# Kernel optimization log

Hardware: AMD Instinct MI355X
Metric: run time of the kernel (lower is better)

Reference implementation:

```python
import jax, jax.numpy as jnp
import numpy as np

B, N, F_IN = 32, 1024, 64   # batch, num_nodes, diffusion_size[0]
K = 3                        # expansion_step
H = 2                        # num_heads
HID, RAW, OUT, CLS = 128, 128, 128, 2
D1, D2 = 128, 128            # diffusion_size[1], diffusion_size[2]
CAT = D1 + RAW               # concat dim fed to attention (h || h_prime) = 256


def setup_inputs() -> dict:
    key = jax.random.key(0)
    ks = jax.random.split(key, 40)
    g = lambda i, shape: jax.random.normal(ks[i], shape, dtype=jnp.float32) * 0.05
    inp = {
        'X': jax.random.normal(ks[0], (B, N, F_IN), dtype=jnp.float32),
        'A': jax.random.uniform(ks[1], (B, N, N), dtype=jnp.float32),
        # transition tensors / mixing weights (only the 2 layers used in forward)
        'T': g(2, (2, K, N, N)),
        'theta': jnp.full((2, K), 1.0 / K, dtype=jnp.float32),
        # raw feature projection
        'W_raw': g(3, (F_IN, RAW)), 'b_raw': jnp.zeros((RAW,), jnp.float32),
        # diffusion layer linears
        'Wd0': g(4, (F_IN, D1)), 'bd0': jnp.zeros((D1,), jnp.float32),
        'Wd1': g(5, (D1, D2)),   'bd1': jnp.zeros((D2,), jnp.float32),
        # final classifier
        'W_fin': g(6, (OUT, CLS)), 'b_fin': jnp.zeros((CLS,), jnp.float32),
    }
    # two CatMultiAttn blocks: q/k/v projections (CAT->HID), out proj (HID->OUT)
    i = 7
    for l in range(2):
        for nm in ('q', 'k', 'v'):
            inp[f'W{nm}{l}'] = g(i, (CAT, HID)); i += 1
            inp[f'b{nm}{l}'] = jnp.zeros((HID,), jnp.float32)
        inp[f'Wo{l}'] = g(i, (HID, OUT)); i += 1
        inp[f'bo{l}'] = jnp.zeros((OUT,), jnp.float32)
    return inp


def _diffusion(theta_l, T_l, h, A, W, b):
    # Q = sum_k theta_k * T_k  (generalized graph diffusion transition)
    Q = jnp.einsum('k,kij->ij', theta_l, T_l)          # [N,N]
    S = Q[None, :, :] * A                               # [B,N,N] mask by adjacency
    z = jnp.einsum('bij,bjf->bif', S, h)                # diffuse features
    return jax.nn.relu(z @ W + b)


def _cat_attn(h, hp, Wq, bq, Wk, bk, Wv, bv, Wo, bo):
    # concatenate diffused + embedding features, multi-head self-attn over nodes
    x = jnp.concatenate([h, hp], axis=-1)               # [B,N,CAT]
    b, n, _ = x.shape
    q = (x @ Wq + bq).reshape(b, n, H, HID // H)
    k = (x @ Wk + bk).reshape(b, n, H, HID // H)
    v = (x @ Wv + bv).reshape(b, n, H, HID // H)
    scale = jnp.asarray(1.0 / np.sqrt(HID // H), x.dtype)
    s = jnp.einsum('bnhd,bmhd->bhnm', q, k) * scale     # [B,H,N,N]
    p = jax.nn.softmax(s, axis=-1)
    ctx = jnp.einsum('bhnm,bmhd->bnhd', p, v).reshape(b, n, HID)
    return jax.nn.relu(ctx @ Wo + bo)


def reference(X, A, T, theta, W_raw, b_raw, Wd0, bd0, Wd1, bd1,
              W_fin, b_fin,
              Wq0, bq0, Wk0, bk0, Wv0, bv0, Wo0, bo0,
              Wq1, bq1, Wk1, bk1, Wv1, bv1, Wo1, bo1):
    theta_soft = jax.nn.softmax(theta, axis=-1)         # [2,K]
    h_prime = X @ W_raw + b_raw                          # [B,N,RAW]
    # layer 0
    h = _diffusion(theta_soft[0], T[0], X, A, Wd0, bd0)  # [B,N,D1]
    h_prime = _cat_attn(h, h_prime, Wq0, bq0, Wk0, bk0, Wv0, bv0, Wo0, bo0)
    # layer 1 (residual fusion)
    h = _diffusion(theta_soft[1], T[1], h, A, Wd1, bd1)  # [B,N,D2]
    h_prime = h_prime + _cat_attn(h, h_prime, Wq1, bq1, Wk1, bk1, Wv1, bv1, Wo1, bo1)
    return h_prime @ W_fin + b_fin                       # [B,N,CLS]
```

## Files before the change

kernel.cpp:

```cpp
#include <hip/hip_runtime.h>
#include <hip/hip_bf16.h>

typedef __hip_bfloat16 bf16;
typedef __attribute__((ext_vector_type(8))) short s8b;
typedef __attribute__((ext_vector_type(4))) short s4b;
typedef __attribute__((ext_vector_type(4))) float f4;
typedef __attribute__((ext_vector_type(4))) float fv4;

#define BB   32
#define NN   1024
#define FIN  64
#define HEADS 2
#define DH   64
#define HIDD 128
#define SZQ  ((size_t)BB * NN * HIDD)

__device__ __forceinline__ ushort f2bf(float x) {
    bf16 h = __float2bfloat16(x);
    return *(ushort*)&h;
}
__device__ __forceinline__ float bfbits2f(ushort h) {
    union { uint u; float f; } c; c.u = (uint)h << 16; return c.f;
}
__device__ __forceinline__ uint pk_bf16(float lo, float hi) {
    return (uint)f2bf(lo) | ((uint)f2bf(hi) << 16);
}
union U8 { short s[8]; s8b v; };
union U4 { short s[4]; s4b v; };
union UQ { ushort u[8]; s8b v; };

__global__ __launch_bounds__(256) void setup_kernel(
        const float* __restrict__ raw, const float* __restrict__ d0,
        const float* __restrict__ d1,
        const float* __restrict__ q0w, const float* __restrict__ k0w,
        const float* __restrict__ v0w, const float* __restrict__ o0w,
        const float* __restrict__ q1w, const float* __restrict__ k1w,
        const float* __restrict__ v1w, const float* __restrict__ o1w,
        ushort* __restrict__ Whi, ushort* __restrict__ Wlo,
        const float* __restrict__ T, const float* __restrict__ theta,
        ushort* __restrict__ Q0hi, ushort* __restrict__ Q0lo,
        ushort* __restrict__ Q1hi, ushort* __restrict__ Q1lo,
        const float* __restrict__ X,
        ushort* __restrict__ XT_hi, ushort* __restrict__ XT_lo) {
    __shared__ float tile[64][65];
    const int bid = blockIdx.x;
    const int t = threadIdx.x;
    if (bid < 1024) {
        int id = bid * 256 + t;
        const float* src; int K, off;
        if      (id <   8192) { src = raw; K =  64; off = 0; }
        else if (id <  16384) { src = d0;  K =  64; off = 8192; }
        else if (id <  32768) { src = d1;  K = 128; off = 16384; }
        else if (id <  65536) { src = q0w; K = 256; off = 32768; }
        else if (id <  98304) { src = k0w; K = 256; off = 65536; }
        else if (id < 131072) { src = v0w; K = 256; off = 98304; }
        else if (id < 147456) { src = o0w; K = 128; off = 131072; }
        else if (id < 180224) { src = q1w; K = 256; off = 147456; }
        else if (id < 212992) { src = k1w; K = 256; off = 180224; }
        else if (id < 245760) { src = v1w; K = 256; off = 212992; }
        else                  { src = o1w; K = 128; off = 245760; }
        int il = id - off;
        int k = il >> 7, c = il & 127;
        float w = src[il];
        ushort h = f2bf(w);
        Whi[off + c * K + k] = h;
        Wlo[off + c * K + k] = f2bf(w - bfbits2f(h));
    } else if (bid < 1536) {
        const int tb = bid - 1024;
        const int b  = tb >> 4;
        const int n0 = (tb & 15) * 64;
        {
            int nl = t >> 2, f0 = (t & 3) * 16;
            const float* xp = X + ((size_t)b * NN + n0 + nl) * 64 + f0;
#pragma unroll
            for (int i = 0; i < 16; i += 4)
                *(float4*)&tile[nl][f0 + i] = *(const float4*)(xp + i);
        }
        __syncthreads();
        {
            int f = t >> 2, n1 = (t & 3) * 16;
            U8 h0, h1, l0, l1;
#pragma unroll
            for (int i = 0; i < 16; i++) {
                float v = tile[n1 + i][f];
                ushort hh = f2bf(v);
                ushort ll = f2bf(v - bfbits2f(hh));
                if (i < 8) { h0.s[i] = (short)hh; l0.s[i] = (short)ll; }
                else       { h1.s[i - 8] = (short)hh; l1.s[i - 8] = (short)ll; }
            }
            size_t gb = ((size_t)b * 64 + f) * NN + n0 + n1;
            *(s8b*)&XT_hi[gb]     = h0.v;  *(s8b*)&XT_hi[gb + 8] = h1.v;
            *(s8b*)&XT_lo[gb]     = l0.v;  *(s8b*)&XT_lo[gb + 8] = l1.v;
        }
    } else {
        const int layer = (bid < 2048) ? 0 : 1;
        ushort* Qhi = layer ? Q1hi : Q0hi;
        ushort* Qlo = layer ? Q1lo : Q0lo;
        float t0 = theta[layer * 3 + 0];
        float t1 = theta[layer * 3 + 1];
        float t2 = theta[layer * 3 + 2];
        float m  = fmaxf(t0, fmaxf(t1, t2));
        float e0 = expf(t0 - m), e1 = expf(t1 - m), e2 = expf(t2 - m);
        float inv = 1.0f / (e0 + e1 + e2);
        e0 *= inv; e1 *= inv; e2 *= inv;
        size_t base = ((size_t)((bid - 1536) & 511) * 256 + t) * 8;
        const float* Tl = T + (size_t)layer * 3 * NN * NN;
        U8 hi, lo;
#pragma unroll
        for (int i = 0; i < 8; i++) {
            float q = e0 * Tl[base + i]
                    + e1 * Tl[base + i + (size_t)NN * NN]
                    + e2 * Tl[base + i + (size_t)2 * NN * NN];
            ushort hh = f2bf(q);
            hi.s[i] = (short)hh;
            lo.s[i] = (short)f2bf(q - bfbits2f(hh));
        }
        *(s8b*)&Qhi[base] = hi.v;
        *(s8b*)&Qlo[base] = lo.v;
    }
}

template<int F, bool WRITE_HT>
__global__ __launch_bounds__(512, 4) void diff_dense_kernel(
        const ushort* __restrict__ Qhi, const ushort* __restrict__ Qlo,
        const float* __restrict__ A,
        const ushort* __restrict__ hT_hi, const ushort* __restrict__ hT_lo,
        const ushort* __restrict__ WT_hi, const ushort* __restrict__ WT_lo,
        const float* __restrict__ bias,
        float* __restrict__ hout,
        ushort* __restrict__ hiT, ushort* __restrict__ loT) {
    constexpr int SS  = 72;
    constexpr int NT  = F / 16;
    constexpr int NCW = NT / 4;
    constexpr int SZ2 = F + 8;
    constexpr int P1 = 2 * 64 * SS + 2 * F * SS;
    constexpr int P2 = 2 * 64 * SZ2 + 2 * 128 * 40;
    __shared__ short smem[(P1 > P2) ? P1 : P2];
    short* Shi = smem;
    short* Slo = Shi + 64 * SS;
    short* Hhi = Slo + 64 * SS;
    short* Hlo = Hhi + (size_t)F * SS;
    short* Zhi = smem;
    short* Zlo = Zhi + 64 * SZ2;
    short* Wsh = Zlo + 64 * SZ2;
    short* Wsl = Wsh + 128 * 40;

    const int bidx = blockIdx.x;
    const int u  = bidx >> 3;
    const int b  = (bidx & 7) + 8 * (u >> 4);
    const int i0 = (u & 15) * 64;
    const int t  = threadIdx.x;
    const int w  = t >> 6, lane = t & 63;
    const int quad = lane >> 4, c = lane & 15;
    const int rh = w >> 2;
    const int ch = w & 3;

    const int srow = t >> 3, scol = (t & 7) * 8;
    const float*  Ap = A   + ((size_t)b * NN + i0 + srow) * NN + scol;
    const ushort* Qh = Qhi + (size_t)(i0 + srow) * NN + scol;
    const ushort* Ql = Qlo + (size_t)(i0 + srow) * NN + scol;
    constexpr int HTR = 512 / F;
    constexpr int HJ  = 64 / HTR;
    constexpr int HV  = HJ / 8;
    const int hrow = t / HTR, hcol = (t % HTR) * HJ;
    const ushort* Hh = hT_hi + ((size_t)b * F + hrow) * NN + hcol;
    const ushort* Hl = hT_lo + ((size_t)b * F + hrow) * NN + hcol;

    f4 acc[2][NCW];
#pragma unroll
    for (int i = 0; i < 2; i++)
#pragma unroll
        for (int j = 0; j < NCW; j++) acc[i][j] = (f4){0.f, 0.f, 0.f, 0.f};

    fv4 a0 = __builtin_nontemporal_load((const fv4*)Ap);
    fv4 a1 = __builtin_nontemporal_load((const fv4*)(Ap + 4));
    s8b hhv[HV], hlv[HV];
#pragma unroll
    for (int vv = 0; vv < HV; vv++) {
        hhv[vv] = *(const s8b*)(Hh + 8 * vv);
        hlv[vv] = *(const s8b*)(Hl + 8 * vv);
    }
    UQ qh, ql;
    qh.v = *(const s8b*)Qh;
    ql.v = *(const s8b*)Ql;

#pragma unroll 1
    for (int j0 = 0; j0 < NN; j0 += 64) {
        __syncthreads();
        {
            float av[8] = {a0[0], a0[1], a0[2], a0[3], a1[0], a1[1], a1[2], a1[3]};
            U8 hi, lo;
#pragma unroll
            for (int i = 0; i < 8; i++) {
                float q = bfbits2f(qh.u[i]) + bfbits2f(ql.u[i]);
                float s = q * av[i];
                ushort hb = f2bf(s);
                hi.s[i] = (short)hb;
                lo.s[i] = (short)f2bf(s - bfbits2f(hb));
            }
            *(s8b*)&Shi[srow * SS + scol] = hi.v;
            *(s8b*)&Slo[srow * SS + scol] = lo.v;
#pragma unroll
            for (int vv = 0; vv < HV; vv++) {
                *(s8b*)&Hhi[hrow * SS + hcol + 8 * vv] = hhv[vv];
                *(s8b*)&Hlo[hrow * SS + hcol + 8 * vv] = hlv[vv];
            }
        }
        __syncthreads();

        if (j0 + 64 < NN) {
            a0 = __builtin_nontemporal_load((const fv4*)(Ap + j0 + 64));
            a1 = __builtin_nontemporal_load((const fv4*)(Ap + j0 + 68));
#pragma unroll
            for (int vv = 0; vv < HV; vv++) {
                hhv[vv] = *(const s8b*)(Hh + j0 + 64 + 8 * vv);
                hlv[vv] = *(const s8b*)(Hl + j0 + 64 + 8 * vv);
            }
            qh.v = *(const s8b*)(Qh + j0 + 64);
            ql.v = *(const s8b*)(Ql + j0 + 64);
        }

#pragma unroll
        for (int ks = 0; ks < 2; ks++) {
            s8b ah0 = *(const s8b*)&Shi[(32 * rh + c) * SS + ks * 32 + quad * 8];
            s8b al0 = *(const s8b*)&Slo[(32 * rh + c) * SS + ks * 32 + quad * 8];
            s8b ah1 = *(const s8b*)&Shi[(32 * rh + 16 + c) * SS + ks * 32 + quad * 8];
            s8b al1 = *(const s8b*)&Slo[(32 * rh + 16 + c) * SS + ks * 32 + quad * 8];
#pragma unroll
            for (int ctn = 0; ctn < NCW; ctn++) {
                const int nt = ch * NCW + ctn;
                s8b bhi = *(const s8b*)&Hhi[(nt * 16 + c) * SS + ks * 32 + quad * 8];
                s8b blo = *(const s8b*)&Hlo[(nt * 16 + c) * SS + ks * 32 + quad * 8];
                acc[0][ctn] = __builtin_amdgcn_mfma_f32_16x16x32_bf16(ah0, bhi, acc[0][ctn], 0, 0, 0);
                acc[0][ctn] = __builtin_amdgcn_mfma_f32_16x16x32_bf16(al0, bhi, acc[0][ctn], 0, 0, 0);
                acc[0][ctn] = __builtin_amdgcn_mfma_f32_16x16x32_bf16(ah0, blo, acc[0][ctn], 0, 0, 0);
                acc[1][ctn] = __builtin_amdgcn_mfma_f32_16x16x32_bf16(ah1, bhi, acc[1][ctn], 0, 0, 0);
                acc[1][ctn] = __builtin_amdgcn_mfma_f32_16x16x32_bf16(al1, bhi, acc[1][ctn], 0, 0, 0);
                acc[1][ctn] = __builtin_amdgcn_mfma_f32_16x16x32_bf16(ah1, blo, acc[1][ctn], 0, 0, 0);
            }
        }
    }

    __syncthreads();
#pragma unroll
    for (int st = 0; st < 2; st++)
#pragma unroll
        for (int ctn = 0; ctn < NCW; ctn++)
#pragma unroll
            for (int r = 0; r < 4; r++) {
                const int row = 32 * rh + 16 * st + quad * 4 + r;
                const int col = (ch * NCW + ctn) * 16 + c;
                float v = acc[st][ctn][r];
                ushort hh = f2bf(v);
                Zhi[row * SZ2 + col] = (short)hh;
                Zlo[row * SZ2 + col] = (short)f2bf(v - bfbits2f(hh));
            }

    const int rh2 = w >> 2;
    const int ch2 = w & 3;
    f4 acc2[2][2];
#pragma unroll
    for (int st = 0; st < 2; st++)
#pragma unroll
        for (int i = 0; i < 2; i++) acc2[st][i] = (f4){0.f, 0.f, 0.f, 0.f};

    constexpr int NKT = F / 32;
    const int wcc = t >> 2, wkk = (t & 3) * 8;
    s8b pwh = *(const s8b*)&WT_hi[(size_t)wcc * F + wkk];
    s8b pwl = *(const s8b*)&WT_lo[(size_t)wcc * F + wkk];
    for (int kt = 0; kt < NKT; kt++) {
        __syncthreads();
        *(s8b*)&Wsh[wcc * 40 + wkk] = pwh;
        *(s8b*)&Wsl[wcc * 40 + wkk] = pwl;
        __syncthreads();
        if (kt + 1 < NKT) {
            size_t gsrc = (size_t)wcc * F + (kt + 1) * 32 + wkk;
            pwh = *(const s8b*)&WT_hi[gsrc];
            pwl = *(const s8b*)&WT_lo[gsrc];
        }

        s8b ah0 = *(const s8b*)&Zhi[(32 * rh2 + c) * SZ2 + kt * 32 + quad * 8];
        s8b al0 = *(const s8b*)&Zlo[(32 * rh2 + c) * SZ2 + kt * 32 + quad * 8];
        s8b ah1 = *(const s8b*)&Zhi[(32 * rh2 + 16 + c) * SZ2 + kt * 32 + quad * 8];
        s8b al1 = *(const s8b*)&Zlo[(32 * rh2 + 16 + c) * SZ2 + kt * 32 + quad * 8];
#pragma unroll
        for (int ct = 0; ct < 2; ct++) {
            s8b bh = *(const s8b*)&Wsh[(ch2 * 32 + ct * 16 + c) * 40 + quad * 8];
            s8b bl = *(const s8b*)&Wsl[(ch2 * 32 + ct * 16 + c) * 40 + quad * 8];
            acc2[0][ct] = __builtin_amdgcn_mfma_f32_16x16x32_bf16(ah0, bh, acc2[0][ct], 0, 0, 0);
            acc2[0][ct] = __builtin_amdgcn_mfma_f32_16x16x32_bf16(al0, bh, acc2[0][ct], 0, 0, 0);
            acc2[0][ct] = __builtin_amdgcn_mfma_f32_16x16x32_bf16(ah0, bl, acc2[0][ct], 0, 0, 0);
            acc2[1][ct] = __builtin_amdgcn_mfma_f32_16x16x32_bf16(ah1, bh, acc2[1][ct], 0, 0, 0);
            acc2[1][ct] = __builtin_amdgcn_mfma_f32_16x16x32_bf16(al1, bh, acc2[1][ct], 0, 0, 0);
            acc2[1][ct] = __builtin_amdgcn_mfma_f32_16x16x32_bf16(ah1, bl, acc2[1][ct], 0, 0, 0);
        }
    }

#pragma unroll
    for (int st = 0; st < 2; st++) {
        const int rg0 = i0 + 32 * rh2 + 16 * st + quad * 4;
#pragma unroll
        for (int ct = 0; ct < 2; ct++) {
            const int col = ch2 * 32 + ct * 16 + c;
            float bv = bias[col];
            float vv[4];
#pragma unroll
            for (int r = 0; r < 4; r++) {
                float v = fmaxf(acc2[st][ct][r] + bv, 0.f);
                hout[((size_t)b * NN + rg0 + r) * 128 + col] = v;
                vv[r] = v;
            }
            if (WRITE_HT) {
                U4 ph, pl;
#pragma unroll
                for (int r = 0; r < 4; r++) {
                    ushort hh = f2bf(vv[r]);
                    ph.s[r] = (short)hh;
                    pl.s[r] = (short)f2bf(vv[r] - bfbits2f(hh));
                }
                size_t tb = ((size_t)b * 128 + col) * NN + rg0;
                *(s4b*)&hiT[tb] = ph.v;
                *(s4b*)&loT[tb] = pl.v;
            }
        }
    }
}

template<int K1, int K2, int CB, bool RELU, bool RESID, int OMODE>
__global__ __launch_bounds__(512) void dense_mfma_kernel(
        const float* __restrict__ in1, const float* __restrict__ in2,
        const ushort* __restrict__ WT_hi, const ushort* __restrict__ WT_lo,
        const float* __restrict__ bias, const float* __restrict__ biask,
        const float* __restrict__ biasv,
        float* __restrict__ out, ushort* __restrict__ outq) {
    constexpr int KD  = K1 + K2;
    constexpr int NKT = KD / 32;
    constexpr int NCH = CB / 32;
    constexpr int WCH = CB * 4;
    constexpr int WPT = (WCH + 511) / 512;
    __shared__ short Xhi[128][40], Xlo[128][40];
    __shared__ short Whi[CB][40], Wlo[CB][40];

    int bx, by;
    if (OMODE == 1) {
        const int xcd = blockIdx.x & 7, qq = blockIdx.x >> 3;
        by = qq & 1;
        bx = ((qq >> 1) << 3) | xcd;
    } else { bx = blockIdx.x; by = blockIdx.y; }
    const int r0 = bx * 128;
    const int c0 = by * CB;
    const int t  = threadIdx.x;
    const int w  = t >> 6, lane = t & 63;
    const int quad = lane >> 4, c = lane & 15;
    const int rh = w >> 1;
    const int ch = w & 1;

    f4 acc[2][NCH];
#pragma unroll
    for (int st = 0; st < 2; st++)
#pragma unroll
        for (int i = 0; i < NCH; i++) acc[st][i] = (f4){0.f, 0.f, 0.f, 0.f};

    const int xrow = t >> 2, xkk = (t & 3) * 8;
    float4 pa, pbq;
    s8b pwh[WPT], pwl[WPT];
    auto loadX = [&](int k0) {
        int g = r0 + xrow;
        const float* p;
        if (K2 > 0) {
            int k = k0 + xkk;
            p = (k < K1) ? (in1 + (size_t)g * K1 + k)
                         : (in2 + (size_t)g * K2 + (k - K1));
        } else {
            p = in1 + (size_t)g * K1 + k0 + xkk;
        }
        pa = *(const float4*)p; pbq = *(const float4*)(p + 4);
    };
    auto loadW = [&](int k0) {
#pragma unroll
        for (int i = 0; i < WPT; i++) {
            int id = t + i * 512;
            if ((WCH % 512 == 0) || id < WCH) {
                int cc = id >> 2, kk = (id & 3) * 8;
                size_t gsrc = (size_t)(c0 + cc) * KD + k0 + kk;
                pwh[i] = *(const s8b*)&WT_hi[gsrc];
                pwl[i] = *(const s8b*)&WT_lo[gsrc];
            }
        }
    };
    loadX(0); loadW(0);

    for (int kt = 0; kt < NKT; kt++) {
        __syncthreads();
        {
            float sv[8] = {pa.x, pa.y, pa.z, pa.w, pbq.x, pbq.y, pbq.z, pbq.w};
            U8 hi, lo;
#pragma unroll
            for (int i = 0; i < 8; i++) {
                ushort hh = f2bf(sv[i]);
                hi.s[i] = (short)hh;
                lo.s[i] = (short)f2bf(sv[i] - bfbits2f(hh));
            }
            *(s8b*)&Xhi[xrow][xkk] = hi.v;
            *(s8b*)&Xlo[xrow][xkk] = lo.v;
        }
        {
#pragma unroll
            for (int i = 0; i < WPT; i++) {
                int id = t + i * 512;
                if ((WCH % 512 == 0) || id < WCH) {
                    int cc = id >> 2, kk = (id & 3) * 8;
                    *(s8b*)&Whi[cc][kk] = pwh[i];
                    *(s8b*)&Wlo[cc][kk] = pwl[i];
                }
            }
        }
        __syncthreads();
        if (kt + 1 < NKT) { loadX(kt * 32 + 32); loadW(kt * 32 + 32); }

        s8b ah0 = *(const s8b*)&Xhi[32 * rh + c][quad * 8];
        s8b al0 = *(const s8b*)&Xlo[32 * rh + c][quad * 8];
        s8b ah1 = *(const s8b*)&Xhi[32 * rh + 16 + c][quad * 8];
        s8b al1 = *(const s8b*)&Xlo[32 * rh + 16 + c][quad * 8];
#pragma unroll
        for (int ct = 0; ct < NCH; ct++) {
            s8b bh = *(const s8b*)&Whi[ch * (CB / 2) + ct * 16 + c][quad * 8];
            s8b bl = *(const s8b*)&Wlo[ch * (CB / 2) + ct * 16 + c][quad * 8];
            acc[0][ct] = __builtin_amdgcn_mfma_f32_16x16x32_bf16(ah0, bh, acc[0][ct], 0, 0, 0);
            acc[0][ct] = __builtin_amdgcn_mfma_f32_16x16x32_bf16(al0, bh, acc[0][ct], 0, 0, 0);
            acc[0][ct] = __builtin_amdgcn_mfma_f32_16x16x32_bf16(ah0, bl, acc[0][ct], 0, 0, 0);
            acc[1][ct] = __builtin_amdgcn_mfma_f32_16x16x32_bf16(ah1, bh, acc[1][ct], 0, 0, 0);
            acc[1][ct] = __builtin_amdgcn_mfma_f32_16x16x32_bf16(al1, bh, acc[1][ct], 0, 0, 0);
            acc[1][ct] = __builtin_amdgcn_mfma_f32_16x16x32_bf16(ah1, bl, acc[1][ct], 0, 0, 0);
        }
    }

#pragma unroll
    for (int st = 0; st < 2; st++) {
        const int row_g0 = r0 + 32 * rh + 16 * st + quad * 4;
#pragma unroll
        for (int ct = 0; ct < NCH; ct++) {
            const int col = c0 + ch * (CB / 2) + ct * 16 + c;
            if (OMODE == 1) {
                int tensor = col >> 7, cc2 = col & 127;
                float bv = (tensor == 0 ? bias : tensor == 1 ? biask : biasv)[cc2];
                int head = cc2 >> 6, d = cc2 & 63;
                int b = row_g0 >> 10, n = row_g0 & 1023;
                if (tensor == 2) {
                    U4 pk;
#pragma unroll
                    for (int r = 0; r < 4; r++) pk.s[r] = (short)f2bf(acc[st][ct][r] + bv);
                    size_t addr = (((size_t)b * HEADS + head) * 64 + d) * NN + n;
                    *(s4b*)&outq[2 * SZQ + addr] = pk.v;
                } else {
                    ushort* dst = outq + (size_t)tensor * SZQ
                                + (((size_t)b * HEADS + head) * NN + n) * 64 + d;
#pragma unroll
                    for (int r = 0; r < 4; r++) dst[(size_t)r * 64] = f2bf(acc[st][ct][r] + bv);
                }
            } else {
                float bv = bias[col];
#pragma unroll
                for (int r = 0; r < 4; r++) {
                    float v = acc[st][ct][r] + bv;
                    if (RELU) v = fmaxf(v, 0.f);
                    size_t o = (size_t)(row_g0 + r) * 128 + col;
                    if (RESID) v += out[o];
                    out[o] = v;
                }
            }
        }
    }
}

template<bool FINAL>
__global__ __launch_bounds__(512) void attn_oproj_kernel(
        const ushort* __restrict__ q, const ushort* __restrict__ k,
        const ushort* __restrict__ vt,
        const ushort* __restrict__ WoT_hi, const ushort* __restrict__ WoT_lo,
        const float* __restrict__ bo,
        float* __restrict__ hp,
        const float* __restrict__ Wfin, const float* __restrict__ bfin,
        float* __restrict__ fout) {
    constexpr int ZS = 136;
    constexpr int PB = 2 * 128 * ZS + 2 * 128 * 40 + 512;
    __shared__ short smem[PB];
    short* Ks  = smem;
    short* Vt  = smem + 128 * 72;
    short* Zhi = smem;
    short* Zlo = Zhi + 128 * ZS;
    short* Wsh = Zlo + 128 * ZS;
    short* Wsl = Wsh + 128 * 40;
    float* red = (float*)(Wsl + 128 * 40);

    const int bidx = blockIdx.x;
    const int u  = bidx >> 3;
    const int b  = (bidx & 7) + 8 * (u >> 3);
    const int n0 = (u & 7) * 128;
    const int t  = threadIdx.x;
    const int w  = t >> 6;
    const int lane = t & 63;
    const int quad = lane >> 4, c = lane & 15;
    const float scale = 0.125f;

    const int skey = t >> 2, sd0 = (t & 3) * 16;
    const int svd  = t >> 3, svc = (t & 7) * 16;

    s8b pk0, pk1, pv0, pv1;
    auto loadKV = [&](size_t base, int kt0) {
        const ushort* kr = k + base + (size_t)(kt0 + skey) * 64 + sd0;
        pk0 = *(const s8b*)kr;
        pk1 = *(const s8b*)(kr + 8);
        const ushort* vr = vt + base + (size_t)svd * NN + kt0 + svc;
        pv0 = *(const s8b*)vr;
        pv1 = *(const s8b*)(vr + 8);
    };

    f4 Oh[2][4];
    float li[2];

#pragma unroll
    for (int h = 0; h < 2; h++) {
        const size_t kvbase = ((size_t)(b * HEADS + h)) * NN * 64;
        s8b qf0, qf1;
        {
            const ushort* qrow = q + kvbase + (size_t)(n0 + 16 * w + c) * 64;
            qf0 = *(const s8b*)(qrow + quad * 8);
            qf1 = *(const s8b*)(qrow + 32 + quad * 8);
        }
        if (h == 0) loadKV(kvbase, 0);
        f4 O[4];
#pragma unroll
        for (int i = 0; i < 4; i++) O[i] = (f4){0.f, 0.f, 0.f, 0.f};
        float l_i = 0.f;

        for (int kt0 = 0; kt0 < NN; kt0 += 128) {
            __syncthreads();
            {
                *(s8b*)&Ks[skey * 72 + sd0]     = pk0;
                *(s8b*)&Ks[skey * 72 + sd0 + 8] = pk1;
                *(s8b*)&Vt[svd * 136 + svc]     = pv0;
                *(s8b*)&Vt[svd * 136 + svc + 8] = pv1;
            }
            __syncthreads();
            if (kt0 + 128 < NN)      loadKV(kvbase, kt0 + 128);
            else if (h == 0)         loadKV(kvbase + (size_t)NN * 64, 0);

            f4 sg[4][2];
#pragma unroll
            for (int g = 0; g < 4; g++) {
                const int kb = g * 32;
                sg[g][0] = (f4){0.f, 0.f, 0.f, 0.f};
                sg[g][1] = (f4){0.f, 0.f, 0.f, 0.f};
#pragma unroll
                for (int ck = 0; ck < 2; ck++) {
                    s8b ka = *(const s8b*)&Ks[(kb + c) * 72 + ck * 32 + quad * 8];
                    s8b kB = *(const s8b*)&Ks[(kb + 16 + c) * 72 + ck * 32 + quad * 8];
                    s8b qf = ck ? qf1 : qf0;
                    sg[g][0] = __builtin_amdgcn_mfma_f32_16x16x32_bf16(ka, qf, sg[g][0], 0, 0, 0);
                    sg[g][1] = __builtin_amdgcn_mfma_f32_16x16x32_bf16(kB, qf, sg[g][1], 0, 0, 0);
                }
            }
            float pv[4][8];
            float ps = 0.f;
#pragma unroll
            for (int g = 0; g < 4; g++)
#pragma unroll
                for (int r = 0; r < 4; r++) {
                    pv[g][r]     = __expf(sg[g][0][r] * scale);
                    pv[g][4 + r] = __expf(sg[g][1][r] * scale);
                    ps += pv[g][r] + pv[g][4 + r];
                }
            ps += __shfl_xor(ps, 16);
            ps += __shfl_xor(ps, 32);
            l_i += ps;

            int addr0 = ((((2 * quad) & 3) << 4) | c) << 2;
            int addr1 = ((((2 * quad + 1) & 3) << 4) | c) << 2;
            int tsel = quad >> 1;
#pragma unroll
            for (int g = 0; g < 4; g++) {
                const int kb = g * 32;
                uint Da01 = pk_bf16(pv[g][0], pv[g][1]), Da23 = pk_bf16(pv[g][2], pv[g][3]);
                uint Db01 = pk_bf16(pv[g][4], pv[g][5]), Db23 = pk_bf16(pv[g][6], pv[g][7]);
                int A01_0 = __builtin_amdgcn_ds_bpermute(addr0, (int)Da01);
                int A23_0 = __builtin_amdgcn_ds_bpermute(addr0, (int)Da23);
                int B01_0 = __builtin_amdgcn_ds_bpermute(addr0, (int)Db01);
                int B23_0 = __builtin_amdgcn_ds_bpermute(addr0, (int)Db23);
                int A01_1 = __builtin_amdgcn_ds_bpermute(addr1, (int)Da01);
                int A23_1 = __builtin_amdgcn_ds_bpermute(addr1, (int)Da23);
                int B01_1 = __builtin_amdgcn_ds_bpermute(addr1, (int)Db01);
                int B23_1 = __builtin_amdgcn_ds_bpermute(addr1, (int)Db23);
                union { int i[4]; s8b s; } pf;
                pf.i[0] = tsel ? B01_0 : A01_0;
                pf.i[1] = tsel ? B23_0 : A23_0;
                pf.i[2] = tsel ? B01_1 : A01_1;
                pf.i[3] = tsel ? B23_1 : A23_1;
#pragma unroll
                for (int dt = 0; dt < 4; dt++) {
                    s8b vf = *(const s8b*)&Vt[(16 * dt + c) * 136 + kb + quad * 8];
                    O[dt] = __builtin_amdgcn_mfma_f32_16x16x32_bf16(vf, pf.s, O[dt], 0, 0, 0);
                }
            }
        }
        li[h] = 1.0f / l_i;
#pragma unroll
        for (int dt = 0; dt < 4; dt++) Oh[h][dt] = O[dt];
    }

    __syncthreads();
    {
        const int zrow = 16 * w + c;
#pragma unroll
        for (int h = 0; h < 2; h++) {
            float inv = li[h];
#pragma unroll
            for (int dt = 0; dt < 4; dt++) {
                U4 ph, pl;
#pragma unroll
                for (int r = 0; r < 4; r++) {
                    float v = Oh[h][dt][r] * inv;
                    ushort hh = f2bf(v);
                    ph.s[r] = (short)hh;
                    pl.s[r] = (short)f2bf(v - bfbits2f(hh));
                }
                int col = h * 64 + 16 * dt + 4 * quad;
                *(s4b*)&Zhi[zrow * ZS + col] = ph.v;
                *(s4b*)&Zlo[zrow * ZS + col] = pl.v;
            }
        }
    }

    const int rh = w >> 1;
    const int ch = w & 1;
    f4 acc[2][4];
#pragma unroll
    for (int st = 0; st < 2; st++)
#pragma unroll
        for (int i = 0; i < 4; i++) acc[st][i] = (f4){0.f, 0.f, 0.f, 0.f};

    const int occ = t >> 2, okk = (t & 3) * 8;
    s8b owh = *(const s8b*)&WoT_hi[(size_t)occ * 128 + okk];
    s8b owl = *(const s8b*)&WoT_lo[(size_t)occ * 128 + okk];
    for (int kt = 0; kt < 4; kt++) {
        __syncthreads();
        *(s8b*)&Wsh[occ * 40 + okk] = owh;
        *(s8b*)&Wsl[occ * 40 + okk] = owl;
        __syncthreads();
        if (kt + 1 < 4) {
            size_t gsrc = (size_t)occ * 128 + (kt + 1) * 32 + okk;
            owh = *(const s8b*)&WoT_hi[gsrc];
            owl = *(const s8b*)&WoT_lo[gsrc];
        }

        s8b ah0 = *(const s8b*)&Zhi[(32 * rh + c) * ZS + kt * 32 + quad * 8];
        s8b al0 = *(const s8b*)&Zlo[(32 * rh + c) * ZS + kt * 32 + quad * 8];
        s8b ah1 = *(const s8b*)&Zhi[(32 * rh + 16 + c) * ZS + kt * 32 + quad * 8];
        s8b al1 = *(const s8b*)&Zlo[(32 * rh + 16 + c) * ZS + kt * 32 + quad * 8];
#pragma unroll
        for (int ct = 0; ct < 4; ct++) {
            s8b bh = *(const s8b*)&Wsh[(ch * 64 + ct * 16 + c) * 40 + quad * 8];
            s8b bl = *(const s8b*)&Wsl[(ch * 64 + ct * 16 + c) * 40 + quad * 8];
            acc[0][ct] = __builtin_amdgcn_mfma_f32_16x16x32_bf16(ah0, bh, acc[0][ct], 0, 0, 0);
            acc[0][ct] = __builtin_amdgcn_mfma_f32_16x16x32_bf16(al0, bh, acc[0][ct], 0, 0, 0);
            acc[0][ct] = __builtin_amdgcn_mfma_f32_16x16x32_bf16(ah0, bl, acc[0][ct], 0, 0, 0);
            acc[1][ct] = __builtin_amdgcn_mfma_f32_16x16x32_bf16(ah1, bh, acc[1][ct], 0, 0, 0);
            acc[1][ct] = __builtin_amdgcn_mfma_f32_16x16x32_bf16(al1, bh, acc[1][ct], 0, 0, 0);
            acc[1][ct] = __builtin_amdgcn_mfma_f32_16x16x32_bf16(ah1, bl, acc[1][ct], 0, 0, 0);
        }
    }

    if (FINAL) {
        float fc[2][2][4];
#pragma unroll
        for (int st = 0; st < 2; st++)
#pragma unroll
            for (int o = 0; o < 2; o++)
#pragma unroll
                for (int r = 0; r < 4; r++) fc[st][o][r] = 0.f;
#pragma unroll
        for (int ct = 0; ct < 4; ct++) {
            const int col = ch * 64 + ct * 16 + c;
            float bv = bo[col];
            float w0 = Wfin[col * 2], w1 = Wfin[col * 2 + 1];
#pragma unroll
            for (int st = 0; st < 2; st++) {
                const size_t rg = (size_t)b * NN + n0 + 32 * rh + 16 * st + quad * 4;
#pragma unroll
                for (int r = 0; r < 4; r++) {
                    float v = fmaxf(acc[st][ct][r] + bv, 0.f);
                    v += hp[(rg + r) * 128 + col];
                    fc[st][0][r] += v * w0;
                    fc[st][1][r] += v * w1;
                }
            }
        }
#pragma unroll
        for (int st = 0; st < 2; st++)
#pragma unroll
            for (int r = 0; r < 4; r++) {
                float a0 = fc[st][0][r], a1 = fc[st][1][r];
#pragma unroll
                for (int off = 1; off < 16; off <<= 1) {
                    a0 += __shfl_xor(a0, off, 16);
                    a1 += __shfl_xor(a1, off, 16);
                }
                fc[st][0][r] = a0; fc[st][1][r] = a1;
            }
        if (ch == 1 && c == 0) {
#pragma unroll
            for (int st = 0; st < 2; st++)
#pragma unroll
                for (int r = 0; r < 4; r++) {
                    int lr = 32 * rh + 16 * st + quad * 4 + r;
                    red[lr * 2]     = fc[st][0][r];
                    red[lr * 2 + 1] = fc[st][1][r];
                }
        }
        __syncthreads();
        if (ch == 0 && c == 0) {
#pragma unroll
            for (int st = 0; st < 2; st++)
#pragma unroll
                for (int r = 0; r < 4; r++) {
                    int lr = 32 * rh + 16 * st + quad * 4 + r;
                    size_t row = (size_t)b * NN + n0 + lr;
                    fout[row * 2]     = fc[st][0][r] + red[lr * 2]     + bfin[0];
                    fout[row * 2 + 1] = fc[st][1][r] + red[lr * 2 + 1] + bfin[1];
                }
        }
        return;
    }

#pragma unroll
    for (int st = 0; st < 2; st++) {
        const size_t rg = (size_t)b * NN + n0 + 32 * rh + 16 * st + quad * 4;
#pragma unroll
        for (int ct = 0; ct < 4; ct++) {
            const int col = ch * 64 + ct * 16 + c;
            float bv = bo[col];
#pragma unroll
            for (int r = 0; r < 4; r++)
                hp[(rg + r) * 128 + col] = fmaxf(acc[st][ct][r] + bv, 0.f);
        }
    }
}

extern "C" void kernel_launch(void* const* d_in, const int* in_sizes, int n_in,
                              void* d_out, int out_size, void* d_ws, size_t ws_size,
                              hipStream_t stream) {
    (void)in_sizes; (void)n_in; (void)out_size; (void)ws_size;
    const float* X     = (const float*)d_in[0];
    const float* A     = (const float*)d_in[1];
    const float* T     = (const float*)d_in[2];
    const float* theta = (const float*)d_in[3];
    const float* W_raw = (const float*)d_in[4];
    const float* b_raw = (const float*)d_in[5];
    const float* Wd0   = (const float*)d_in[6];
    const float* bd0   = (const float*)d_in[7];
    const float* Wd1   = (const float*)d_in[8];
    const float* bd1   = (const float*)d_in[9];
    const float* W_fin = (const float*)d_in[10];
    const float* b_fin = (const float*)d_in[11];
    const float* Wq0 = (const float*)d_in[12]; const float* bq0 = (const float*)d_in[13];
    const float* Wk0 = (const float*)d_in[14]; const float* bk0 = (const float*)d_in[15];
    const float* Wv0 = (const float*)d_in[16]; const float* bv0 = (const float*)d_in[17];
    const float* Wo0 = (const float*)d_in[18]; const float* bo0 = (const float*)d_in[19];
    const float* Wq1 = (const float*)d_in[20]; const float* bq1 = (const float*)d_in[21];
    const float* Wk1 = (const float*)d_in[22]; const float* bk1 = (const float*)d_in[23];
    const float* Wv1 = (const float*)d_in[24]; const float* bv1 = (const float*)d_in[25];
    const float* Wo1 = (const float*)d_in[26]; const float* bo1 = (const float*)d_in[27];

    float* ws   = (float*)d_ws;
    const size_t SZ = (size_t)BB * NN * HIDD;
    ushort* Q0hi = (ushort*)ws;
    ushort* Q0lo = Q0hi + (size_t)NN * NN;
    float* hp   = ws + (size_t)NN * NN;
    float* h    = hp + SZ;
    float* z    = h + SZ;
    ushort* qb  = (ushort*)(z + SZ);
    ushort* kb  = qb + SZ;
    ushort* XT_hi = qb + 3 * SZ;
    ushort* XT_lo = XT_hi + SZ / 2;
    ushort* hT_hi = XT_lo + SZ / 2;
    ushort* hT_lo = hT_hi + SZ;
    ushort* WT_hi = hT_lo + SZ;
    ushort* WT_lo = WT_hi + 262144;
    ushort* Q1hi = WT_lo + 262144;
    ushort* Q1lo = Q1hi + (size_t)NN * NN;

    const int OFF_RAW = 0, OFF_D0 = 8192, OFF_D1 = 16384, OFF_QKV0 = 32768,
              OFF_O0 = 131072, OFF_QKV1 = 147456, OFF_O1 = 245760;

    const int attnGrid = BB * (NN / 128);
    const int diffGrid = BB * (NN / 64);
    const dim3 dg1(256, 1);

    setup_kernel<<<2560, 256, 0, stream>>>(W_raw, Wd0, Wd1, Wq0, Wk0, Wv0, Wo0,
                                           Wq1, Wk1, Wv1, Wo1, WT_hi, WT_lo,
                                           T, theta, Q0hi, Q0lo, Q1hi, Q1lo,
                                           X, XT_hi, XT_lo);

    dense_mfma_kernel<64, 0, 128, false, false, 0><<<dg1, 512, 0, stream>>>(
        X, nullptr, WT_hi + OFF_RAW, WT_lo + OFF_RAW, b_raw, nullptr, nullptr,
        hp, nullptr);
    diff_dense_kernel<64, true><<<diffGrid, 512, 0, stream>>>(
        Q0hi, Q0lo, A, XT_hi, XT_lo, WT_hi + OFF_D0, WT_lo + OFF_D0, bd0,
        h, hT_hi, hT_lo);
    dense_mfma_kernel<128, 128, 192, false, false, 1><<<512, 512, 0, stream>>>(
        h, hp, WT_hi + OFF_QKV0, WT_lo + OFF_QKV0, bq0, bk0, bv0,
        nullptr, qb);
    attn_oproj_kernel<false><<<attnGrid, 512, 0, stream>>>(
        qb, kb, qb + 2 * SZ, WT_hi + OFF_O0, WT_lo + OFF_O0, bo0,
        hp, nullptr, nullptr, nullptr);

    diff_dense_kernel<128, false><<<diffGrid, 512, 0, stream>>>(
        Q1hi, Q1lo, A, hT_hi, hT_lo, WT_hi + OFF_D1, WT_lo + OFF_D1, bd1,
        h, nullptr, nullptr);
    dense_mfma_kernel<128, 128, 192, false, false, 1><<<512, 512, 0, stream>>>(
        h, hp, WT_hi + OFF_QKV1, WT_lo + OFF_QKV1, bq1, bk1, bv1,
        nullptr, qb);
    attn_oproj_kernel<true><<<attnGrid, 512, 0, stream>>>(
        qb, kb, qb + 2 * SZ, WT_hi + OFF_O1, WT_lo + OFF_O1, bo1,
        hp, W_fin, b_fin, (float*)d_out);
}
```

Baseline: 506.1 us.

## Double diffusion kernel row tile to 128 and split the epilogue into two passes

Each diffusion block now covers 128 node rows instead of 64, which halves the grid and halves the number of times the h^T tiles are reloaded per batch. Warps are rearranged to 4 row groups by 2 column groups, so each warp holds more accumulators. The second linear-layer epilogue runs in two 64-row passes that reuse the shared Z buffer. The A loads also drop the nontemporal hint and use plain float4 loads through a prefetch lambda. Register pressure grows and occupancy may drop under launch_bounds(512,4).

Measured after the change: 531.3 us. 1.05x slower.

```diff
diff --git a/kernel.cpp b/kernel.cpp
--- a/kernel.cpp
+++ b/kernel.cpp
@@ -5,7 +5,6 @@
 typedef __attribute__((ext_vector_type(8))) short s8b;
 typedef __attribute__((ext_vector_type(4))) short s4b;
 typedef __attribute__((ext_vector_type(4))) float f4;
-typedef __attribute__((ext_vector_type(4))) float fv4;
 
 #define BB   32
 #define NN   1024
@@ -130,15 +129,14 @@
         float* __restrict__ hout,
         ushort* __restrict__ hiT, ushort* __restrict__ loT) {
     constexpr int SS  = 72;
-    constexpr int NT  = F / 16;
-    constexpr int NCW = NT / 4;
-    constexpr int SZ2 = F + 8;
-    constexpr int P1 = 2 * 64 * SS + 2 * F * SS;
+    constexpr int NCW = F / 32;
+    constexpr int SZ2 = (F == 64) ? 72 : 136;
+    constexpr int P1 = 2 * 128 * SS + 2 * F * SS;
     constexpr int P2 = 2 * 64 * SZ2 + 2 * 128 * 40;
     __shared__ short smem[(P1 > P2) ? P1 : P2];
     short* Shi = smem;
-    short* Slo = Shi + 64 * SS;
-    short* Hhi = Slo + 64 * SS;
+    short* Slo = Shi + 128 * SS;
+    short* Hhi = Slo + 128 * SS;
     short* Hlo = Hhi + (size_t)F * SS;
     short* Zhi = smem;
     short* Zlo = Zhi + 64 * SZ2;
@@ -147,15 +145,15 @@
 
     const int bidx = blockIdx.x;
     const int u  = bidx >> 3;
-    const int b  = (bidx & 7) + 8 * (u >> 4);
-    const int i0 = (u & 15) * 64;
+    const int b  = (bidx & 7) + 8 * (u >> 3);
+    const int i0 = (u & 7) * 128;
     const int t  = threadIdx.x;
     const int w  = t >> 6, lane = t & 63;
     const int quad = lane >> 4, c = lane & 15;
-    const int rh = w >> 2;
-    const int ch = w & 3;
-
-    const int srow = t >> 3, scol = (t & 7) * 8;
+    const int rh = w >> 1;
+    const int ch = w & 1;
+
+    const int srow = t >> 2, scol = (t & 3) * 16;
     const float*  Ap = A   + ((size_t)b * NN + i0 + srow) * NN + scol;
     const ushort* Qh = Qhi + (size_t)(i0 + srow) * NN + scol;
     const ushort* Ql = Qlo + (size_t)(i0 + srow) * NN + scol;
@@ -172,53 +170,62 @@
 #pragma unroll
         for (int j = 0; j < NCW; j++) acc[i][j] = (f4){0.f, 0.f, 0.f, 0.f};
 
-    fv4 a0 = __builtin_nontemporal_load((const fv4*)Ap);
-    fv4 a1 = __builtin_nontemporal_load((const fv4*)(Ap + 4));
-    s8b hhv[HV], hlv[HV];
-#pragma unroll
-    for (int vv = 0; vv < HV; vv++) {
-        hhv[vv] = *(const s8b*)(Hh + 8 * vv);
-        hlv[vv] = *(const s8b*)(Hl + 8 * vv);
-    }
-    UQ qh, ql;
-    qh.v = *(const s8b*)Qh;
-    ql.v = *(const s8b*)Ql;
+    float4 pa[4];
+    UQ pqh[2], pql[2];
+    s8b phh[HV], phl[HV];
+    auto loadTile = [&](int j0) {
+#pragma unroll
+        for (int k = 0; k < 4; k++) pa[k] = *(const float4*)(Ap + j0 + 4 * k);
+#pragma unroll
+        for (int k = 0; k < 2; k++) {
+            pqh[k].v = *(const s8b*)(Qh + j0 + 8 * k);
+            pql[k].v = *(const s8b*)(Ql + j0 + 8 * k);
+        }
+#pragma unroll
+        for (int vv = 0; vv < HV; vv++) {
+            phh[vv] = *(const s8b*)(Hh + j0 + 8 * vv);
+            phl[vv] = *(const s8b*)(Hl + j0 + 8 * vv);
+        }
+    };
+    loadTile(0);
 
 #pragma unroll 1
     for (int j0 = 0; j0 < NN; j0 += 64) {
         __syncthreads();
         {
-            float av[8] = {a0[0], a0[1], a0[2], a0[3], a1[0], a1[1], a1[2], a1[3]};
-            U8 hi, lo;
+            float av[16] = {pa[0].x, pa[0].y, pa[0].z, pa[0].w,
+                            pa[1].x, pa[1].y, pa[1].z, pa[1].w,
+                            pa[2].x, pa[2].y, pa[2].z, pa[2].w,
+                            pa[3].x, pa[3].y, pa[3].z, pa[3].w};
+            U8 h0, h1, l0, l1;
 #pragma unroll
             for (int i = 0; i < 8; i++) {
-                float q = bfbits2f(qh.u[i]) + bfbits2f(ql.u[i]);
+                float q = bfbits2f(pqh[0].u[i]) + bfbits2f(pql[0].u[i]);
                 float s = q * av[i];
                 ushort hb = f2bf(s);
-                hi.s[i] = (short)hb;
-                lo.s[i] = (short)f2bf(s - bfbits2f(hb));
-            }
-            *(s8b*)&Shi[srow * SS + scol] = hi.v;
-            *(s8b*)&Slo[srow * SS + scol] = lo.v;
+                h0.s[i] = (short)hb;
+                l0.s[i] = (short)f2bf(s - bfbits2f(hb));
+            }
+#pragma unroll
+            for (int i = 0; i < 8; i++) {
+                float q = bfbits2f(pqh[1].u[i]) + bfbits2f(pql[1].u[i]);
+                float s = q * av[8 + i];
+                ushort hb = f2bf(s);
+                h1.s[i] = (short)hb;
+                l1.s[i] = (short)f2bf(s - bfbits2f(hb));
+            }
+            *(s8b*)&Shi[srow * SS + scol]     = h0.v;
+            *(s8b*)&Shi[srow * SS + scol + 8] = h1.v;
+            *(s8b*)&Slo[srow * SS + scol]     = l0.v;
+            *(s8b*)&Slo[srow * SS + scol + 8] = l1.v;
 #pragma unroll
             for (int vv = 0; vv < HV; vv++) {
-                *(s8b*)&Hhi[hrow * SS + hcol + 8 * vv] = hhv[vv];
-                *(s8b*)&Hlo[hrow * SS + hcol + 8 * vv] = hlv[vv];
+                *(s8b*)&Hhi[hrow * SS + hcol + 8 * vv] = phh[vv];
+                *(s8b*)&Hlo[hrow * SS + hcol + 8 * vv] = phl[vv];
             }
         }
         __syncthreads();
-
-        if (j0 + 64 < NN) {
-            a0 = __builtin_nontemporal_load((const fv4*)(Ap + j0 + 64));
-            a1 = __builtin_nontemporal_load((const fv4*)(Ap + j0 + 68));
-#pragma unroll
-            for (int vv = 0; vv < HV; vv++) {
-                hhv[vv] = *(const s8b*)(Hh + j0 + 64 + 8 * vv);
-                hlv[vv] = *(const s8b*)(Hl + j0 + 64 + 8 * vv);
-            }
-            qh.v = *(const s8b*)(Qh + j0 + 64);
-            ql.v = *(const s8b*)(Ql + j0 + 64);
-        }
+        if (j0 + 64 < NN) loadTile(j0 + 64);
 
 #pragma unroll
         for (int ks = 0; ks < 2; ks++) {
@@ -241,86 +248,91 @@
         }
     }
 
-    __syncthreads();
-#pragma unroll
-    for (int st = 0; st < 2; st++)
-#pragma unroll
-        for (int ctn = 0; ctn < NCW; ctn++)
-#pragma unroll
-            for (int r = 0; r < 4; r++) {
-                const int row = 32 * rh + 16 * st + quad * 4 + r;
-                const int col = (ch * NCW + ctn) * 16 + c;
-                float v = acc[st][ctn][r];
-                ushort hh = f2bf(v);
-                Zhi[row * SZ2 + col] = (short)hh;
-                Zlo[row * SZ2 + col] = (short)f2bf(v - bfbits2f(hh));
-            }
-
+    constexpr int NKT = F / 32;
     const int rh2 = w >> 2;
     const int ch2 = w & 3;
-    f4 acc2[2][2];
-#pragma unroll
-    for (int st = 0; st < 2; st++)
-#pragma unroll
-        for (int i = 0; i < 2; i++) acc2[st][i] = (f4){0.f, 0.f, 0.f, 0.f};
-
-    constexpr int NKT = F / 32;
     const int wcc = t >> 2, wkk = (t & 3) * 8;
-    s8b pwh = *(const s8b*)&WT_hi[(size_t)wcc * F + wkk];
-    s8b pwl = *(const s8b*)&WT_lo[(size_t)wcc * F + wkk];
-    for (int kt = 0; kt < NKT; kt++) {
+
+#pragma unroll 1
+    for (int p = 0; p < 2; p++) {
         __syncthreads();
-        *(s8b*)&Wsh[wcc * 40 + wkk] = pwh;
-        *(s8b*)&Wsl[wcc * 40 + wkk] = pwl;
-        __syncthreads();
-        if (kt + 1 < NKT) {
-            size_t gsrc = (size_t)wcc * F + (kt + 1) * 32 + wkk;
-            pwh = *(const s8b*)&WT_hi[gsrc];
-            pwl = *(const s8b*)&WT_lo[gsrc];
-        }
-
-        s8b ah0 = *(const s8b*)&Zhi[(32 * rh2 + c) * SZ2 + kt * 32 + quad * 8];
-        s8b al0 = *(const s8b*)&Zlo[(32 * rh2 + c) * SZ2 + kt * 32 + quad * 8];
-        s8b ah1 = *(const s8b*)&Zhi[(32 * rh2 + 16 + c) * SZ2 + kt * 32 + quad * 8];
-        s8b al1 = *(const s8b*)&Zlo[(32 * rh2 + 16 + c) * SZ2 + kt * 32 + quad * 8];
-#pragma unroll
-        for (int ct = 0; ct < 2; ct++) {
-            s8b bh = *(const s8b*)&Wsh[(ch2 * 32 + ct * 16 + c) * 40 + quad * 8];
-            s8b bl = *(const s8b*)&Wsl[(ch2 * 32 + ct * 16 + c) * 40 + quad * 8];
-            acc2[0][ct] = __builtin_amdgcn_mfma_f32_16x16x32_bf16(ah0, bh, acc2[0][ct], 0, 0, 0);
-            acc2[0][ct] = __builtin_amdgcn_mfma_f32_16x16x32_bf16(al0, bh, acc2[0][ct], 0, 0, 0);
-            acc2[0][ct] = __builtin_amdgcn_mfma_f32_16x16x32_bf16(ah0, bl, acc2[0][ct], 0, 0, 0);
-            acc2[1][ct] = __builtin_amdgcn_mfma_f32_16x16x32_bf16(ah1, bh, acc2[1][ct], 0, 0, 0);
-            acc2[1][ct] = __builtin_amdgcn_mfma_f32_16x16x32_bf16(al1, bh, acc2[1][ct], 0, 0, 0);
-            acc2[1][ct] = __builtin_amdgcn_mfma_f32_16x16x32_bf16(ah1, bl, acc2[1][ct], 0, 0, 0);
-        }
-    }
-
-#pragma unroll
-    for (int st = 0; st < 2; st++) {
-        const int rg0 = i0 + 32 * rh2 + 16 * st + quad * 4;
-#pragma unroll
-        for (int ct = 0; ct < 2; ct++) {
-            const int col = ch2 * 32 + ct * 16 + c;
-            float bv = bias[col];
-            float vv[4];
-#pragma unroll
-            for (int r = 0; r < 4; r++) {
-                float v = fmaxf(acc2[st][ct][r] + bv, 0.f);
-                hout[((size_t)b * NN + rg0 + r) * 128 + col] = v;
-                vv[r] = v;
-            }
-            if (WRITE_HT) {
-                U4 ph, pl;
+        if ((rh >> 1) == p) {
+#pragma unroll
+            for (int st = 0; st < 2; st++)
+#pragma unroll
+                for (int ctn = 0; ctn < NCW; ctn++)
+#pragma unroll
+                    for (int r = 0; r < 4; r++) {
+                        const int row = 32 * (rh & 1) + 16 * st + quad * 4 + r;
+                        const int col = (ch * NCW + ctn) * 16 + c;
+                        float v = acc[st][ctn][r];
+                        ushort hh = f2bf(v);
+                        Zhi[row * SZ2 + col] = (short)hh;
+                        Zlo[row * SZ2 + col] = (short)f2bf(v - bfbits2f(hh));
+                    }
+        }
+        f4 acc2[2][2];
+#pragma unroll
+        for (int st = 0; st < 2; st++)
+#pragma unroll
+            for (int i = 0; i < 2; i++) acc2[st][i] = (f4){0.f, 0.f, 0.f, 0.f};
+
+        s8b pwh = *(const s8b*)&WT_hi[(size_t)wcc * F + wkk];
+        s8b pwl = *(const s8b*)&WT_lo[(size_t)wcc * F + wkk];
+        for (int kt = 0; kt < NKT; kt++) {
+            __syncthreads();
+            *(s8b*)&Wsh[wcc * 40 + wkk] = pwh;
+            *(s8b*)&Wsl[wcc * 40 + wkk] = pwl;
+            __syncthreads();
+            if (kt + 1 < NKT) {
+                size_t gsrc = (size_t)wcc * F + (kt + 1) * 32 + wkk;
+                pwh = *(const s8b*)&WT_hi[gsrc];
+                pwl = *(const s8b*)&WT_lo[gsrc];
+            }
+
+            s8b ah0 = *(const s8b*)&Zhi[(32 * rh2 + c) * SZ2 + kt * 32 + quad * 8];
+            s8b al0 = *(const s8b*)&Zlo[(32 * rh2 + c) * SZ2 + kt * 32 + quad * 8];
+            s8b ah1 = *(const s8b*)&Zhi[(32 * rh2 + 16 + c) * SZ2 + kt * 32 + quad * 8];
+            s8b al1 = *(const s8b*)&Zlo[(32 * rh2 + 16 + c) * SZ2 + kt * 32 + quad * 8];
+#pragma unroll
+            for (int ct = 0; ct < 2; ct++) {
+                s8b bh = *(const s8b*)&Wsh[(ch2 * 32 + ct * 16 + c) * 40 + quad * 8];
+                s8b bl = *(const s8b*)&Wsl[(ch2 * 32 + ct * 16 + c) * 40 + quad * 8];
+                acc2[0][ct] = __builtin_amdgcn_mfma_f32_16x16x32_bf16(ah0, bh, acc2[0][ct], 0, 0, 0);
+                acc2[0][ct] = __builtin_amdgcn_mfma_f32_16x16x32_bf16(al0, bh, acc2[0][ct], 0, 0, 0);
+                acc2[0][ct] = __builtin_amdgcn_mfma_f32_16x16x32_bf16(ah0, bl, acc2[0][ct], 0, 0, 0);
+                acc2[1][ct] = __builtin_amdgcn_mfma_f32_16x16x32_bf16(ah1, bh, acc2[1][ct], 0, 0, 0);
+                acc2[1][ct] = __builtin_amdgcn_mfma_f32_16x16x32_bf16(al1, bh, acc2[1][ct], 0, 0, 0);
+                acc2[1][ct] = __builtin_amdgcn_mfma_f32_16x16x32_bf16(ah1, bl, acc2[1][ct], 0, 0, 0);
+            }
+        }
+
+#pragma unroll
+        for (int st = 0; st < 2; st++) {
+            const int rg0 = i0 + 64 * p + 32 * rh2 + 16 * st + quad * 4;
+#pragma unroll
+            for (int ct = 0; ct < 2; ct++) {
+                const int col = ch2 * 32 + ct * 16 + c;
+                float bv = bias[col];
+                float vv[4];
 #pragma unroll
                 for (int r = 0; r < 4; r++) {
-                    ushort hh = f2bf(vv[r]);
-                    ph.s[r] = (short)hh;
-                    pl.s[r] = (short)f2bf(vv[r] - bfbits2f(hh));
-                }
-                size_t tb = ((size_t)b * 128 + col) * NN + rg0;
-                *(s4b*)&hiT[tb] = ph.v;
-                *(s4b*)&loT[tb] = pl.v;
+                    float v = fmaxf(acc2[st][ct][r] + bv, 0.f);
+                    hout[((size_t)b * NN + rg0 + r) * 128 + col] = v;
+                    vv[r] = v;
+                }
+                if (WRITE_HT) {
+                    U4 ph, pl;
+#pragma unroll
+                    for (int r = 0; r < 4; r++) {
+                        ushort hh = f2bf(vv[r]);
+                        ph.s[r] = (short)hh;
+                        pl.s[r] = (short)f2bf(vv[r] - bfbits2f(hh));
+                    }
+                    size_t tb = ((size_t)b * 128 + col) * NN + rg0;
+                    *(s4b*)&hiT[tb] = ph.v;
+                    *(s4b*)&loT[tb] = pl.v;
+                }
             }
         }
     }
@@ -793,7 +805,7 @@
               OFF_O0 = 131072, OFF_QKV1 = 147456, OFF_O1 = 245760;
 
     const int attnGrid = BB * (NN / 128);
-    const int diffGrid = BB * (NN / 64);
+    const int diffGrid = BB * (NN / 128);
     const dim3 dg1(256, 1);
 
     setup_kernel<<<2560, 256, 0, stream>>>(W_raw, Wd0, Wd1, Wq0, Wk0, Wv0, Wo0,
```
